# Kernel optimization log

Measured on AMD Instinct MI355X. Metric: run time of the kernel, lower is better.

## Reference

```python
import jax, jax.numpy as jnp
import numpy as np
from jax import lax

B, N, T, D, H, O = 64, 16, 64, 128, 256, 1  # batch, max_neighbors, time_steps, input_dim, hidden_dim, output_dim
NEG = -1e30


def gru(x, h0, Wih, Whh, bih, bhh):
    """Single-layer PyTorch-convention GRU. x:(B,T,D) h0:(B,H) -> (ys:(B,T,H), hT:(B,H))."""
    def step(h, xt):
        gi = xt @ Wih.T + bih          # (B,3H)
        gh = h @ Whh.T + bhh           # (B,3H)
        i_r, i_z, i_n = jnp.split(gi, 3, axis=-1)
        h_r, h_z, h_n = jnp.split(gh, 3, axis=-1)
        r = jax.nn.sigmoid(i_r + h_r)
        z = jax.nn.sigmoid(i_z + h_z)
        n = jnp.tanh(i_n + r * h_n)
        h_new = (1.0 - z) * n + z * h
        return h_new, h_new
    hT, ys = lax.scan(step, h0, jnp.swapaxes(x, 0, 1))
    return jnp.swapaxes(ys, 0, 1), hT


def setup_inputs() -> dict:
    key = jax.random.key(0)
    ks = jax.random.split(key, 16)
    def xavier(k, shape):
        fan_out, fan_in = shape[0], shape[1]
        std = np.sqrt(2.0 / (fan_in + fan_out))
        return jax.random.normal(k, shape, dtype=jnp.float32) * std
    inp = {
        "node_input": jax.random.normal(ks[0], (B, T, D), dtype=jnp.float32),
        "node_hidden": jnp.zeros((1, B, H), dtype=jnp.float32),
        "neighbors_input": jax.random.normal(ks[1], (B, N, T, D), dtype=jnp.float32),
        "neighbors_hidden": jnp.zeros((1, B * N, H), dtype=jnp.float32),
        "s_len": jax.random.randint(ks[2], (B,), 1, T + 1),
        # Node GRU params
        "Wih_node": xavier(ks[3], (3 * H, D)),
        "Whh_node": xavier(ks[4], (3 * H, H)),
        "bih_node": jnp.zeros((3 * H,), dtype=jnp.float32),
        "bhh_node": jnp.zeros((3 * H,), dtype=jnp.float32),
        # Neighbor GRU params
        "Wih_ngh": xavier(ks[5], (3 * H, D)),
        "Whh_ngh": xavier(ks[6], (3 * H, H)),
        "bih_ngh": jnp.zeros((3 * H,), dtype=jnp.float32),
        "bhh_ngh": jnp.zeros((3 * H,), dtype=jnp.float32),
        # Attention projections (torch Linear convention: y = x @ W.T)
        "Wq": xavier(ks[7], (H, H)),
        "Wk": xavier(ks[8], (H, H)),
        "Wv": xavier(ks[9], (H, H)),
        "Wbil": xavier(ks[10], (H, H)),
        "bbil": jnp.zeros((T,), dtype=jnp.float32),
        "Wprj": xavier(ks[11], (O, H)),
        "bprj": jnp.zeros((O,), dtype=jnp.float32),
    }
    return inp


def reference(node_input, node_hidden, neighbors_input, neighbors_hidden, s_len,
              Wih_node, Whh_node, bih_node, bhh_node,
              Wih_ngh, Whh_ngh, bih_ngh, bhh_ngh,
              Wq, Wk, Wv, Wbil, bbil, Wprj, bprj):
    # --- GRU encodes (nlayers=1) ---
    node_out, node_hT = gru(node_input, node_hidden[0], Wih_node, Whh_node, bih_node, bhh_node)  # (B,T,H)
    ngh_in = neighbors_input.reshape(B * N, T, D)
    ngh_out, ngh_hT = gru(ngh_in, neighbors_hidden[0], Wih_ngh, Whh_ngh, bih_ngh, bhh_ngh)
    ngh_out = ngh_out.reshape(B, N, T, H)

    # --- Time attention, batched over all N+1 slots (instead of python loop) ---
    kv = jnp.concatenate([node_out[:, None], ngh_out], axis=1)  # (B,M,T,H), M=N+1
    Q = node_out @ Wq.T                                          # (B,T,H) shared query for all slots
    K = kv @ Wk.T                                                # (B,M,T,H)
    V = kv @ Wv.T                                                # (B,M,T,H)
    # Bilinear score: (Q @ Wbil) @ K^T + b  -> (B,M,T,T); bbil:(T,) broadcasts on last axis
    S = jnp.einsum('bth,bmsh->bmts', Q @ Wbil, K) + bbil
    causal = jnp.triu(jnp.ones((T, T), dtype=bool), k=1)         # mask future positions
    S = jnp.where(causal, NEG, S)
    A = jax.nn.softmax(S, axis=-1)                               # (B,M,T,T); dropout=0 (eval)
    ctx = jnp.einsum('bmts,bmsh->bmth', A, V)                    # (B,M,T,H)

    # --- Output projection and sum over slots ---
    proj = ctx @ Wprj.T + bprj                                   # (B,M,T,O)
    out = jnp.sum(proj.reshape(B, N + 1, T * O), axis=1)         # (B,T*O)
    out = jnp.squeeze(out)
    return out, node_hT[None], ngh_hT[None], A
```

## Files before the change

kernel.cpp:

```cpp
#include <hip/hip_runtime.h>
#include <hip/hip_bf16.h>

#define NEGV -1e30f
typedef __attribute__((ext_vector_type(8))) short bf16x8;
typedef __attribute__((ext_vector_type(4))) float f32x4;

__device__ __forceinline__ float rcpf_(float x) { return __builtin_amdgcn_rcpf(x); }
__device__ __forceinline__ float sigmoidf_(float x) { return rcpf_(1.0f + __expf(-x)); }
__device__ __forceinline__ float tanhf_(float x) {
    float ax = fabsf(x);
    float e = __expf(-2.0f * ax);
    float t = (1.0f - e) * rcpf_(1.0f + e);
    return copysignf(t, x);
}
__device__ __forceinline__ float bf2f(unsigned short u) {
    union { float f; unsigned int i; } x; x.i = ((unsigned int)u) << 16; return x.f;
}
__device__ __forceinline__ float bfsel(uint2 v, int rg) {
    unsigned int w = (rg < 2) ? v.x : v.y;
    return bf2f((unsigned short)((rg & 1) ? (w >> 16) : (w & 0xffffu)));
}

__device__ __forceinline__ void swz_store(const float* __restrict__ src,
    __hip_bfloat16* __restrict__ dst, int idx, int kshift)
{
    int n = idx >> kshift, k = idx & ((1 << kshift) - 1);
    int nt = n >> 4, kt = k >> 5, quad = (k & 31) >> 3, pos = k & 7;
    dst[((size_t)((nt << (kshift - 5)) + kt) * 64 + quad * 16 + (n & 15)) * 8 + pos] =
        (__hip_bfloat16)src[idx];
}

__device__ __forceinline__ void swz_store_g(const float* __restrict__ src,
    __hip_bfloat16* __restrict__ dst, int idx, int kshift)
{
    int n = idx >> kshift, k = idx & ((1 << kshift) - 1);
    int gate = n >> 8, c = n & 255, w = c >> 5, half = (c >> 4) & 1;
    int tileG = w * 6 + gate * 2 + half;
    int kt = k >> 5, quad = (k & 31) >> 3, pos = k & 7;
    dst[((size_t)((tileG << (kshift - 5)) + kt) * 64 + quad * 16 + (n & 15)) * 8 + pos] =
        (__hip_bfloat16)src[idx];
}

__global__ __launch_bounds__(256) void convert_all(
    const float* __restrict__ Wih_n, const float* __restrict__ Wih_g,
    const float* __restrict__ Whh_n, const float* __restrict__ Whh_g,
    const float* __restrict__ Wk_,   const float* __restrict__ Wv_,
    const float* __restrict__ Wbil_, const float* __restrict__ Wq_,
    __hip_bfloat16* Wih_n_sw, __hip_bfloat16* Wih_g_sw,
    __hip_bfloat16* Whh_n_sw, __hip_bfloat16* Whh_g_sw,
    __hip_bfloat16* Wk_sw, __hip_bfloat16* Wv_sw, __hip_bfloat16* wqb_sw)
{
    __shared__ __align__(16) float As[32 * 68];
    __shared__ __align__(16) float Bs[32 * 68];
    if (blockIdx.x < 2816) {
        int g = blockIdx.x * 256 + threadIdx.x;
        if (g < 98304)        swz_store_g(Wih_n, Wih_n_sw, g, 7);
        else if (g < 196608)  swz_store_g(Wih_g, Wih_g_sw, g - 98304, 7);
        else if (g < 393216)  swz_store_g(Whh_n, Whh_n_sw, g - 196608, 8);
        else if (g < 589824)  swz_store_g(Whh_g, Whh_g_sw, g - 393216, 8);
        else if (g < 655360)  swz_store(Wk_,   Wk_sw,   g - 589824, 8);
        else                  swz_store(Wv_,   Wv_sw,   g - 655360, 8);
        return;
    }
    const int bx = blockIdx.x - 2816;
    const int tid = threadIdx.x, tx = tid & 15, ty = tid >> 4;
    const int rb = (bx >> 2) * 64, cb = (bx & 3) * 64;
    float acc[4][4] = {};
    for (int k0 = 0; k0 < 256; k0 += 32) {
        __syncthreads();
        for (int f = tid; f < 2048; f += 256) {
            int kk = f >> 6, r = f & 63;
            As[kk * 68 + r] = Wbil_[(size_t)(k0 + kk) * 256 + rb + r];
        }
        for (int f = tid; f < 2048; f += 256) {
            int kk = f >> 6, c = f & 63;
            Bs[kk * 68 + c] = Wq_[(size_t)(k0 + kk) * 256 + cb + c];
        }
        __syncthreads();
#pragma unroll
        for (int kk = 0; kk < 32; ++kk) {
            float4 a4 = *(const float4*)(As + kk * 68 + ty * 4);
            float4 b4 = *(const float4*)(Bs + kk * 68 + tx * 4);
            float av[4] = {a4.x, a4.y, a4.z, a4.w};
            float bv[4] = {b4.x, b4.y, b4.z, b4.w};
#pragma unroll
            for (int i = 0; i < 4; ++i)
#pragma unroll
                for (int j = 0; j < 4; ++j) acc[i][j] += av[i] * bv[j];
        }
    }
#pragma unroll
    for (int i = 0; i < 4; ++i)
#pragma unroll
        for (int j = 0; j < 4; ++j) {
            int n = rb + ty * 4 + i, k = cb + tx * 4 + j;
            int nt = n >> 4, kt = k >> 5, quad = (k & 31) >> 3, pos = k & 7;
            wqb_sw[((size_t)(nt * 8 + kt) * 64 + quad * 16 + (n & 15)) * 8 + pos] =
                (__hip_bfloat16)acc[i][j];
        }
}

__global__ __launch_bounds__(512) void gi_gemm(
    const float* __restrict__ node_input, const float* __restrict__ neighbors_input,
    const __hip_bfloat16* __restrict__ Wih_n_sw, const __hip_bfloat16* __restrict__ Wih_g_sw,
    const float* __restrict__ bih_node, const float* __restrict__ bhh_node,
    const float* __restrict__ bih_ngh,  const float* __restrict__ bhh_ngh,
    __hip_bfloat16* __restrict__ gi)
{
    __shared__ __align__(16) __hip_bfloat16 xs[64 * 136];
    const int tid = threadIdx.x, wave = tid >> 6, lane = tid & 63;
    const int quad = lane >> 4, lr = lane & 15;
    const int sblk = blockIdx.x >> 4, tc = blockIdx.x & 15;
    const bool isnode = (sblk < 4);
    const float* __restrict__ xb = isnode
        ? (node_input + (size_t)sblk * 16 * 64 * 128)
        : (neighbors_input + ((size_t)sblk * 16 - 64) * 64 * 128);
    const __hip_bfloat16* __restrict__ Wsw = isnode ? Wih_n_sw : Wih_g_sw;
    const float* __restrict__ bi = isnode ? bih_node : bih_ngh;
    const float* __restrict__ bh = isnode ? bhh_node : bhh_ngh;

    bf16x8 wfr[24];
#pragma unroll
    for (int nt = 0; nt < 6; ++nt)
#pragma unroll
        for (int kt = 0; kt < 4; ++kt)
            wfr[nt * 4 + kt] = *(const bf16x8*)(const void*)(
                Wsw + ((size_t)((wave * 6 + nt) * 4 + kt) * 64 + lane) * 8);

    float bias6[6];
#pragma unroll
    for (int tl = 0; tl < 6; ++tl) {
        int gate = tl >> 1;
        int col = gate * 256 + wave * 32 + (tl & 1) * 16 + lr;
        bias6[tl] = bi[col] + (gate < 2 ? bh[col] : 0.0f);
    }

    {
        const int vr = tid >> 3, c0 = (tid & 7) * 16;
        const int r = vr >> 2, tt = vr & 3;
        const float* src = xb + ((size_t)r * 64 + tc * 4 + tt) * 128 + c0;
        float4 v0 = *(const float4*)(src);
        float4 v1 = *(const float4*)(src + 4);
        float4 v2 = *(const float4*)(src + 8);
        float4 v3 = *(const float4*)(src + 12);
        float vv[16] = {v0.x, v0.y, v0.z, v0.w, v1.x, v1.y, v1.z, v1.w,
                        v2.x, v2.y, v2.z, v2.w, v3.x, v3.y, v3.z, v3.w};
        __hip_bfloat16* d = xs + vr * 136 + c0;
#pragma unroll
        for (int j = 0; j < 16; ++j) d[j] = (__hip_bfloat16)vv[j];
    }
    __syncthreads();

    __hip_bfloat16* __restrict__ gout =
        gi + (size_t)((sblk * 8 + wave) * 6) * 16384 + (size_t)lane * 4;

#pragma unroll
    for (int tt = 0; tt < 4; ++tt) {
        int t = tc * 4 + tt;
        bf16x8 afr[4];
#pragma unroll
        for (int kt = 0; kt < 4; ++kt)
            afr[kt] = *(const bf16x8*)(const void*)(xs + (lr * 4 + tt) * 136 + kt * 32 + quad * 8);

#pragma unroll
        for (int tl = 0; tl < 6; ++tl) {
            f32x4 acc = {0.f, 0.f, 0.f, 0.f};
#pragma unroll
            for (int kt = 0; kt < 4; ++kt)
                acc = __builtin_amdgcn_mfma_f32_16x16x32_bf16(afr[kt], wfr[tl * 4 + kt], acc, 0, 0, 0);
            union { __hip_bfloat16 p[4]; uint2 u; } pu;
#pragma unroll
            for (int rg = 0; rg < 4; ++rg) pu.p[rg] = (__hip_bfloat16)(acc[rg] + bias6[tl]);
            *(uint2*)(void*)(gout + (size_t)tl * 16384 + (size_t)t * 256) = pu.u;
        }
    }
}

__global__ __launch_bounds__(512, 2) void scan_kernel(
    const __hip_bfloat16* __restrict__ gi,
    const __hip_bfloat16* __restrict__ Whh_n_sw,
    const __hip_bfloat16* __restrict__ Whh_g_sw,
    const float* __restrict__ bhh_node, const float* __restrict__ bhh_ngh,
    const float* __restrict__ node_hidden, const float* __restrict__ neighbors_hidden,
    __hip_bfloat16* __restrict__ node_out, __hip_bfloat16* __restrict__ ngh_out,
    float* __restrict__ out_node_hT, float* __restrict__ out_ngh_hT)
{
    __shared__ __align__(16) __hip_bfloat16 wlds[96 * 64 * 8];
    __shared__ __align__(16) __hip_bfloat16 hfr[2 * 4096];
    const int tid = threadIdx.x;
    const int wave = tid >> 6, lane = tid & 63;
    const int quad = lane >> 4, lr = lane & 15;
    const int row0 = blockIdx.x * 16;
    const bool isnode = (row0 < 64);
    const __hip_bfloat16* __restrict__ Wsw = isnode ? Whh_n_sw : Whh_g_sw;
    const float* __restrict__ bhh = isnode ? bhh_node : bhh_ngh;

    bf16x8 wreg[36];
#pragma unroll
    for (int nt = 0; nt < 6; ++nt)
#pragma unroll
        for (int kt = 0; kt < 6; ++kt)
            wreg[nt * 6 + kt] = *(const bf16x8*)(const void*)(
                Wsw + ((size_t)((wave * 6 + nt) * 8 + kt) * 64 + lane) * 8);

    for (int f = tid; f < 6144; f += 512) {
        int chunk = f >> 6, l = f & 63;
        int tileG = chunk >> 1, s = chunk & 1;
        *(uint4*)(void*)(wlds + ((size_t)chunk * 64 + l) * 8) =
            *(const uint4*)(const void*)(Wsw + ((size_t)(tileG * 8 + 6 + s) * 64 + l) * 8);
    }

    const __hip_bfloat16* __restrict__ gbase =
        gi + (size_t)((blockIdx.x * 8 + wave) * 6) * 16384 + (size_t)lane * 4;

    const float bhn0 = bhh[512 + wave * 32 + lr];
    const float bhn1 = bhh[512 + wave * 32 + 16 + lr];

    const int hwoff = (wave * 64 + (lr >> 3) * 16 + quad * 4) * 8 + (lr & 7);
    float hreg[8];
    {
        const float* hsrc = isnode ? (node_hidden + (size_t)row0 * 256)
                                   : (neighbors_hidden + (size_t)(row0 - 64) * 256);
#pragma unroll
        for (int half = 0; half < 2; ++half)
#pragma unroll
            for (int rg = 0; rg < 4; ++rg) {
                float v = hsrc[(size_t)(quad * 4 + rg) * 256 + wave * 32 + half * 16 + lr];
                hreg[half * 4 + rg] = v;
                hfr[hwoff + half * 256 + rg * 8] = (__hip_bfloat16)v;
            }
    }

    __hip_bfloat16* optr;
    {
        int orow = tid & 15;
        int ocol = (tid >> 6) * 32 + ((tid >> 4) & 3) * 8;
        optr = isnode ? (node_out + ((size_t)(row0 + orow) * 64) * 256 + ocol)
                      : (ngh_out + ((size_t)(row0 - 64 + orow) * 64) * 256 + ocol);
    }

    uint2 gv[6];
#pragma unroll
    for (int tl = 0; tl < 6; ++tl)
        gv[tl] = *(const uint2*)(const void*)(gbase + (size_t)tl * 16384);

    __syncthreads();

#pragma unroll 1
    for (int t = 0; t < 64; ++t) {
        const __hip_bfloat16* hr = hfr + (t & 1) * 4096;

        const int tp = (t < 63) ? (t + 1) : 63;
        uint2 gvn[6];
#pragma unroll
        for (int tl = 0; tl < 6; ++tl)
            gvn[tl] = *(const uint2*)(const void*)(gbase + (size_t)tl * 16384 + tp * 256);

        if (t) {
            uint4 ov = *(const uint4*)(const void*)(hr + tid * 8);
            *(uint4*)(void*)optr = ov;
            optr += 256;
        }

        f32x4 acc[6] = {{0.f,0.f,0.f,0.f},{0.f,0.f,0.f,0.f},{0.f,0.f,0.f,0.f},
                        {0.f,0.f,0.f,0.f},{0.f,0.f,0.f,0.f},{0.f,0.f,0.f,0.f}};
        {
#pragma unroll
            for (int kt = 0; kt < 3; ++kt) {
                bf16x8 av = *(const bf16x8*)(const void*)(hr + (kt * 64 + lane) * 8);
#pragma unroll
                for (int tl = 0; tl < 6; ++tl)
                    acc[tl] = __builtin_amdgcn_mfma_f32_16x16x32_bf16(av, wreg[tl * 6 + kt], acc[tl], 0, 0, 0);
            }
        }
        {
#pragma unroll
            for (int kt = 3; kt < 6; ++kt) {
                bf16x8 av = *(const bf16x8*)(const void*)(hr + (kt * 64 + lane) * 8);
#pragma unroll
                for (int tl = 0; tl < 6; ++tl)
                    acc[tl] = __builtin_amdgcn_mfma_f32_16x16x32_bf16(av, wreg[tl * 6 + kt], acc[tl], 0, 0, 0);
            }
        }
        {
#pragma unroll
            for (int s = 0; s < 2; ++s) {
                bf16x8 av = *(const bf16x8*)(const void*)(hr + ((6 + s) * 64 + lane) * 8);
#pragma unroll
                for (int tl = 0; tl < 6; ++tl) {
                    bf16x8 bfr = *(const bf16x8*)(const void*)(
                        wlds + ((size_t)((wave * 6 + tl) * 2 + s) * 64 + lane) * 8);
                    acc[tl] = __builtin_amdgcn_mfma_f32_16x16x32_bf16(av, bfr, acc[tl], 0, 0, 0);
                }
            }
        }

        __hip_bfloat16* hw = hfr + ((t + 1) & 1) * 4096 + hwoff;
#pragma unroll
        for (int half = 0; half < 2; ++half) {
            const float bhn = half ? bhn1 : bhn0;
#pragma unroll
            for (int rg = 0; rg < 4; ++rg) {
                float ghr = acc[half][rg];
                float ghz = acc[2 + half][rg];
                float ghn = acc[4 + half][rg] + bhn;
                float gir = bfsel(gv[half], rg);
                float giz = bfsel(gv[2 + half], rg);
                float gin = bfsel(gv[4 + half], rg);
                float r = sigmoidf_(gir + ghr);
                float z = sigmoidf_(giz + ghz);
                float n = tanhf_(gin + r * ghn);
                float hn = (1.0f - z) * n + z * hreg[half * 4 + rg];
                hreg[half * 4 + rg] = hn;
                hw[half * 256 + rg * 8] = (__hip_bfloat16)hn;
            }
        }
#pragma unroll
        for (int tl = 0; tl < 6; ++tl) gv[tl] = gvn[tl];

        asm volatile("s_waitcnt lgkmcnt(0)" ::: "memory");
        __builtin_amdgcn_s_barrier();
        __builtin_amdgcn_sched_barrier(0);
    }

    {
        uint4 ov = *(const uint4*)(const void*)(hfr + tid * 8);
        *(uint4*)(void*)optr = ov;
    }
    {
        float* hdst = isnode ? (out_node_hT + (size_t)row0 * 256)
                             : (out_ngh_hT + (size_t)(row0 - 64) * 256);
#pragma unroll
        for (int half = 0; half < 2; ++half)
#pragma unroll
            for (int rg = 0; rg < 4; ++rg)
                hdst[(size_t)(quad * 4 + rg) * 256 + wave * 32 + half * 16 + lr] = hreg[half * 4 + rg];
    }
}

__global__ __launch_bounds__(256) void q_gemm(
    const __hip_bfloat16* __restrict__ A0,
    const __hip_bfloat16* __restrict__ wqb_sw,
    __hip_bfloat16* __restrict__ Qb)
{
    __shared__ __align__(16) __hip_bfloat16 As[64 * 264];
    const int tid = threadIdx.x, wave = tid >> 6, lane = tid & 63;
    const int quad = lane >> 4, lr = lane & 15;
    const int rb = blockIdx.x * 64;
    const __hip_bfloat16* A = A0 + (size_t)rb * 256;

    for (int f = tid; f < 2048; f += 256) {
        int row = f >> 5, cc = (f & 31) * 8;
        *(uint4*)(void*)(As + row * 264 + cc) =
            *(const uint4*)(const void*)(A + (size_t)row * 256 + cc);
    }
    __syncthreads();

    bf16x8 afr[8];
#pragma unroll
    for (int kt = 0; kt < 8; ++kt)
        afr[kt] = *(const bf16x8*)(const void*)(As + (wave * 16 + lr) * 264 + kt * 32 + quad * 8);

    const int s0 = wave * 16 + quad * 4;
    for (int ntg = 0; ntg < 16; ++ntg) {
        f32x4 acc = {0.f, 0.f, 0.f, 0.f};
#pragma unroll
        for (int kt = 0; kt < 8; ++kt) {
            bf16x8 bfr = *(const bf16x8*)(const void*)(wqb_sw + ((size_t)(ntg * 8 + kt) * 64 + lane) * 8);
            acc = __builtin_amdgcn_mfma_f32_16x16x32_bf16(afr[kt], bfr, acc, 0, 0, 0);
        }
        int col = ntg * 16 + lr;
#pragma unroll
        for (int rg = 0; rg < 4; ++rg)
            Qb[(size_t)(rb + s0 + rg) * 256 + col] = (__hip_bfloat16)acc[rg];
    }
}

__global__ __launch_bounds__(256) void attn_fused(
    const __hip_bfloat16* __restrict__ node_out_b,
    const __hip_bfloat16* __restrict__ ngh_out_b,
    const __hip_bfloat16* __restrict__ Wk_sw, const __hip_bfloat16* __restrict__ Wv_sw,
    const __hip_bfloat16* __restrict__ Qb, const float* __restrict__ bbil,
    const float* __restrict__ Wprj, const float* __restrict__ bprj,
    float* __restrict__ A_out, float* __restrict__ out)
{
    __shared__ __align__(16) __hip_bfloat16 KA[64 * 264];
    __shared__ __align__(16) float Sbuf[64 * 68];
    __shared__ __align__(16) __hip_bfloat16 Pb[64 * 72];
    __shared__ float rowmax[64], rowrcp[64];
    __shared__ float red[64 * 16];
    const int tid = threadIdx.x;
    const int wave = tid >> 6, lane = tid & 63;
    const int quad = lane >> 4, lr = lane & 15;
    const int bm = blockIdx.x, b = bm / 17, m = bm % 17;
    const __hip_bfloat16* __restrict__ A = (m == 0)
        ? (node_out_b + (size_t)b * 64 * 256)
        : (ngh_out_b + ((size_t)(b * 16 + m - 1) * 64) * 256);

    for (int f = tid; f < 2048; f += 256) {
        int row = f >> 5, cc = (f & 31) * 8;
        *(uint4*)(void*)(KA + row * 264 + cc) =
            *(const uint4*)(const void*)(A + (size_t)row * 256 + cc);
    }
    __syncthreads();

    bf16x8 afr[8];
#pragma unroll
    for (int kt = 0; kt < 8; ++kt)
        afr[kt] = *(const bf16x8*)(const void*)(KA + (wave * 16 + lr) * 264 + kt * 32 + quad * 8);
    const __hip_bfloat16* Qrow = Qb + (size_t)b * 64 * 256;
    bf16x8 qfr[8];
#pragma unroll
    for (int kt = 0; kt < 8; ++kt)
        qfr[kt] = *(const bf16x8*)(const void*)(Qrow + (size_t)(wave * 16 + lr) * 256 + kt * 32 + quad * 8);
    __syncthreads();

    {
        const int s0 = wave * 16 + quad * 4;
        for (int ntg = 0; ntg < 16; ++ntg) {
            f32x4 acc = {0.f, 0.f, 0.f, 0.f};
#pragma unroll
            for (int kt = 0; kt < 8; ++kt) {
                bf16x8 bfr = *(const bf16x8*)(const void*)(Wk_sw + ((size_t)(ntg * 8 + kt) * 64 + lane) * 8);
                acc = __builtin_amdgcn_mfma_f32_16x16x32_bf16(afr[kt], bfr, acc, 0, 0, 0);
            }
            int col = ntg * 16 + lr;
#pragma unroll
            for (int rg = 0; rg < 4; ++rg)
                KA[(s0 + rg) * 264 + col] = (__hip_bfloat16)acc[rg];
        }
    }
    __syncthreads();

    f32x4 sacc[4] = {{0.f,0.f,0.f,0.f},{0.f,0.f,0.f,0.f},{0.f,0.f,0.f,0.f},{0.f,0.f,0.f,0.f}};
#pragma unroll
    for (int kt = 0; kt < 8; ++kt) {
#pragma unroll
        for (int c = 0; c < 4; ++c) {
            bf16x8 bfr = *(const bf16x8*)(const void*)(KA + (c * 16 + lr) * 264 + kt * 32 + quad * 8);
            sacc[c] = __builtin_amdgcn_mfma_f32_16x16x32_bf16(qfr[kt], bfr, sacc[c], 0, 0, 0);
        }
    }
#pragma unroll
    for (int c = 0; c < 4; ++c)
#pragma unroll
        for (int rg = 0; rg < 4; ++rg) {
            int t_ = wave * 16 + quad * 4 + rg, s_ = c * 16 + lr;
            Sbuf[t_ * 68 + s_] = (s_ <= t_) ? (sacc[c][rg] + bbil[s_]) : NEGV;
        }
    __syncthreads();

    {
        const int kt2 = wave >> 1;
        const int lp = ((wave & 1) * 2 + (quad >> 1)) * 16 + lr;
        const int j0 = (quad & 1) * 4;
        for (int ntg = 0; ntg < 16; ++ntg) {
            f32x4 acc = {0.f, 0.f, 0.f, 0.f};
#pragma unroll
            for (int kt = 0; kt < 8; ++kt) {
                bf16x8 bfr = *(const bf16x8*)(const void*)(Wv_sw + ((size_t)(ntg * 8 + kt) * 64 + lane) * 8);
                acc = __builtin_amdgcn_mfma_f32_16x16x32_bf16(afr[kt], bfr, acc, 0, 0, 0);
            }
            __hip_bfloat16 t4[4];
#pragma unroll
            for (int rg = 0; rg < 4; ++rg) t4[rg] = (__hip_bfloat16)acc[rg];
            *(uint2*)(void*)(KA + (size_t)(((ntg * 2 + kt2) * 64 + lp) * 8 + j0)) =
                *(const uint2*)(const void*)t4;
        }
    }
    if (tid < 64) {
        float mx = -3.0e38f;
        for (int s = 0; s < 64; ++s) mx = fmaxf(mx, Sbuf[tid * 68 + s]);
        float sum = 0.0f;
        for (int s = 0; s < 64; ++s) sum += __expf(Sbuf[tid * 68 + s] - mx);
        rowmax[tid] = mx;
        rowrcp[tid] = 1.0f / sum;
    }
    __syncthreads();

    for (int idx = tid; idx < 4096; idx += 256) {
        int t_ = idx >> 6, s_ = idx & 63;
        float e = __expf(Sbuf[t_ * 68 + s_] - rowmax[t_]) * rowrcp[t_];
        A_out[(size_t)bm * 4096 + idx] = e;
        Pb[t_ * 72 + s_] = (__hip_bfloat16)e;
    }
    __syncthreads();

    bf16x8 pfr[2];
#pragma unroll
    for (int k2 = 0; k2 < 2; ++k2)
        pfr[k2] = *(const bf16x8*)(const void*)(Pb + (wave * 16 + lr) * 72 + k2 * 32 + quad * 8);
    float part[4] = {0.f, 0.f, 0.f, 0.f};
#pragma unroll
    for (int nt = 0; nt < 16; ++nt) {
        f32x4 cacc = {0.f, 0.f, 0.f, 0.f};
#pragma unroll
        for (int k2 = 0; k2 < 2; ++k2) {
            bf16x8 bfr = *(const bf16x8*)(const void*)(KA + (size_t)((nt * 2 + k2) * 64 + lane) * 8);
            cacc = __builtin_amdgcn_mfma_f32_16x16x32_bf16(pfr[k2], bfr, cacc, 0, 0, 0);
        }
        float wp = Wprj[nt * 16 + lr];
#pragma unroll
        for (int rg = 0; rg < 4; ++rg) part[rg] += cacc[rg] * wp;
    }
#pragma unroll
    for (int rg = 0; rg < 4; ++rg) red[(wave * 16 + quad * 4 + rg) * 16 + lr] = part[rg];
    __syncthreads();
    if (tid < 64) {
        float s = 0.0f;
#pragma unroll
        for (int q = 0; q < 16; ++q) s += red[tid * 16 + q];
        if (m == 0) s += 17.0f * bprj[0];
        atomicAdd(out + b * 64 + tid, s);
    }
}

extern "C" void kernel_launch(void* const* d_in, const int* in_sizes, int n_in,
                              void* d_out, int out_size, void* d_ws, size_t ws_size,
                              hipStream_t stream)
{
    const float* node_input       = (const float*)d_in[0];
    const float* node_hidden      = (const float*)d_in[1];
    const float* neighbors_input  = (const float*)d_in[2];
    const float* neighbors_hidden = (const float*)d_in[3];
    const float* Wih_node = (const float*)d_in[5];
    const float* Whh_node = (const float*)d_in[6];
    const float* bih_node = (const float*)d_in[7];
    const float* bhh_node = (const float*)d_in[8];
    const float* Wih_ngh  = (const float*)d_in[9];
    const float* Whh_ngh  = (const float*)d_in[10];
    const float* bih_ngh  = (const float*)d_in[11];
    const float* bhh_ngh  = (const float*)d_in[12];
    const float* Wq   = (const float*)d_in[13];
    const float* Wk   = (const float*)d_in[14];
    const float* Wv   = (const float*)d_in[15];
    const float* Wbil = (const float*)d_in[16];
    const float* bbil = (const float*)d_in[17];
    const float* Wprj = (const float*)d_in[18];
    const float* bprj = (const float*)d_in[19];

    float* out         = (float*)d_out;
    float* out_node_hT = out + 4096;
    float* out_ngh_hT  = out + 20480;
    float* out_A       = out + 282624;

    char* w = (char*)d_ws;
    __hip_bfloat16* Wih_n_sw = (__hip_bfloat16*)(w + 262144);
    __hip_bfloat16* Wih_g_sw = (__hip_bfloat16*)(w + 458752);
    __hip_bfloat16* Whh_n_sw = (__hip_bfloat16*)(w + 655360);
    __hip_bfloat16* Whh_g_sw = (__hip_bfloat16*)(w + 1048576);
    __hip_bfloat16* Wk_sw    = (__hip_bfloat16*)(w + 1441792);
    __hip_bfloat16* Wv_sw    = (__hip_bfloat16*)(w + 1572864);
    __hip_bfloat16* wqb_sw   = (__hip_bfloat16*)(w + 1703936);
    __hip_bfloat16* node_out_b = (__hip_bfloat16*)(w + 1835008);
    __hip_bfloat16* ngh_out_b  = (__hip_bfloat16*)(w + 3932160);
    __hip_bfloat16* qb_b       = (__hip_bfloat16*)(w + 37486592);
    __hip_bfloat16* gi         = (__hip_bfloat16*)(w + 39583744);

    hipMemsetAsync(d_out, 0, 4096 * sizeof(float), stream);

    convert_all<<<2832, 256, 0, stream>>>(
        Wih_node, Wih_ngh, Whh_node, Whh_ngh, Wk, Wv, Wbil, Wq,
        Wih_n_sw, Wih_g_sw, Whh_n_sw, Whh_g_sw, Wk_sw, Wv_sw, wqb_sw);

    gi_gemm<<<1088, 512, 0, stream>>>(
        node_input, neighbors_input, Wih_n_sw, Wih_g_sw,
        bih_node, bhh_node, bih_ngh, bhh_ngh, gi);

    scan_kernel<<<68, 512, 0, stream>>>(gi, Whh_n_sw, Whh_g_sw,
        bhh_node, bhh_ngh, node_hidden, neighbors_hidden,
        node_out_b, ngh_out_b, out_node_hT, out_ngh_hT);

    q_gemm<<<64, 256, 0, stream>>>(node_out_b, wqb_sw, qb_b);

    attn_fused<<<1088, 256, 0, stream>>>(
        node_out_b, ngh_out_b, Wk_sw, Wv_sw, qb_b, bbil, Wprj, bprj,
        out_A, out);
}
```

Measured before the change: 393.9 us.

## Fold Wk into query side so attention skips per-slot K projection

After: 413.1 us. +4.9%, slower.

```diff
diff --git a/kernel.cpp b/kernel.cpp
--- a/kernel.cpp
+++ b/kernel.cpp
@@ -48,7 +48,8 @@
     const float* __restrict__ Wbil_, const float* __restrict__ Wq_,
     __hip_bfloat16* Wih_n_sw, __hip_bfloat16* Wih_g_sw,
     __hip_bfloat16* Whh_n_sw, __hip_bfloat16* Whh_g_sw,
-    __hip_bfloat16* Wk_sw, __hip_bfloat16* Wv_sw, __hip_bfloat16* wqb_sw)
+    __hip_bfloat16* Wk_sw, __hip_bfloat16* Wv_sw, __hip_bfloat16* wqb_sw,
+    __hip_bfloat16* Wk_t_sw)
 {
     __shared__ __align__(16) float As[32 * 68];
     __shared__ __align__(16) float Bs[32 * 68];
@@ -62,7 +63,16 @@
         else                  swz_store(Wv_,   Wv_sw,   g - 655360, 8);
         return;
     }
-    const int bx = blockIdx.x - 2816;
+    if (blockIdx.x < 3072) {
+        int g = (blockIdx.x - 2816) * 256 + threadIdx.x;
+        int k = g >> 8, n = g & 255;
+        float v = Wk_[(size_t)k * 256 + n];
+        int nt = n >> 4, kt = k >> 5, quad = (k & 31) >> 3, pos = k & 7;
+        Wk_t_sw[((size_t)(nt * 8 + kt) * 64 + quad * 16 + (n & 15)) * 8 + pos] =
+            (__hip_bfloat16)v;
+        return;
+    }
+    const int bx = blockIdx.x - 3072;
     const int tid = threadIdx.x, tx = tid & 15, ty = tid >> 4;
     const int rb = (bx >> 2) * 64, cb = (bx & 3) * 64;
     float acc[4][4] = {};
@@ -341,7 +351,8 @@
 __global__ __launch_bounds__(256) void q_gemm(
     const __hip_bfloat16* __restrict__ A0,
     const __hip_bfloat16* __restrict__ wqb_sw,
-    __hip_bfloat16* __restrict__ Qb)
+    const __hip_bfloat16* __restrict__ Wk_t_sw,
+    __hip_bfloat16* __restrict__ G)
 {
     __shared__ __align__(16) __hip_bfloat16 As[64 * 264];
     const int tid = threadIdx.x, wave = tid >> 6, lane = tid & 63;
@@ -360,6 +371,7 @@
 #pragma unroll
     for (int kt = 0; kt < 8; ++kt)
         afr[kt] = *(const bf16x8*)(const void*)(As + (wave * 16 + lr) * 264 + kt * 32 + quad * 8);
+    __syncthreads();
 
     const int s0 = wave * 16 + quad * 4;
     for (int ntg = 0; ntg < 16; ++ntg) {
@@ -372,15 +384,33 @@
         int col = ntg * 16 + lr;
 #pragma unroll
         for (int rg = 0; rg < 4; ++rg)
-            Qb[(size_t)(rb + s0 + rg) * 256 + col] = (__hip_bfloat16)acc[rg];
+            As[(s0 + rg) * 264 + col] = (__hip_bfloat16)acc[rg];
+    }
+    __syncthreads();
+
+    bf16x8 qfr[8];
+#pragma unroll
+    for (int kt = 0; kt < 8; ++kt)
+        qfr[kt] = *(const bf16x8*)(const void*)(As + (wave * 16 + lr) * 264 + kt * 32 + quad * 8);
+    for (int ntg = 0; ntg < 16; ++ntg) {
+        f32x4 acc = {0.f, 0.f, 0.f, 0.f};
+#pragma unroll
+        for (int kt = 0; kt < 8; ++kt) {
+            bf16x8 bfr = *(const bf16x8*)(const void*)(Wk_t_sw + ((size_t)(ntg * 8 + kt) * 64 + lane) * 8);
+            acc = __builtin_amdgcn_mfma_f32_16x16x32_bf16(qfr[kt], bfr, acc, 0, 0, 0);
+        }
+        int col = ntg * 16 + lr;
+#pragma unroll
+        for (int rg = 0; rg < 4; ++rg)
+            G[(size_t)(rb + s0 + rg) * 256 + col] = (__hip_bfloat16)acc[rg];
     }
 }
 
 __global__ __launch_bounds__(256) void attn_fused(
     const __hip_bfloat16* __restrict__ node_out_b,
     const __hip_bfloat16* __restrict__ ngh_out_b,
-    const __hip_bfloat16* __restrict__ Wk_sw, const __hip_bfloat16* __restrict__ Wv_sw,
-    const __hip_bfloat16* __restrict__ Qb, const float* __restrict__ bbil,
+    const __hip_bfloat16* __restrict__ Wv_sw,
+    const __hip_bfloat16* __restrict__ G, const float* __restrict__ bbil,
     const float* __restrict__ Wprj, const float* __restrict__ bprj,
     float* __restrict__ A_out, float* __restrict__ out)
 {
@@ -408,29 +438,11 @@
 #pragma unroll
     for (int kt = 0; kt < 8; ++kt)
         afr[kt] = *(const bf16x8*)(const void*)(KA + (wave * 16 + lr) * 264 + kt * 32 + quad * 8);
-    const __hip_bfloat16* Qrow = Qb + (size_t)b * 64 * 256;
-    bf16x8 qfr[8];
+    const __hip_bfloat16* Grow = G + (size_t)b * 64 * 256;
+    bf16x8 gfr[8];
 #pragma unroll
     for (int kt = 0; kt < 8; ++kt)
-        qfr[kt] = *(const bf16x8*)(const void*)(Qrow + (size_t)(wave * 16 + lr) * 256 + kt * 32 + quad * 8);
-    __syncthreads();
-
-    {
-        const int s0 = wave * 16 + quad * 4;
-        for (int ntg = 0; ntg < 16; ++ntg) {
-            f32x4 acc = {0.f, 0.f, 0.f, 0.f};
-#pragma unroll
-            for (int kt = 0; kt < 8; ++kt) {
-                bf16x8 bfr = *(const bf16x8*)(const void*)(Wk_sw + ((size_t)(ntg * 8 + kt) * 64 + lane) * 8);
-                acc = __builtin_amdgcn_mfma_f32_16x16x32_bf16(afr[kt], bfr, acc, 0, 0, 0);
-            }
-            int col = ntg * 16 + lr;
-#pragma unroll
-            for (int rg = 0; rg < 4; ++rg)
-                KA[(s0 + rg) * 264 + col] = (__hip_bfloat16)acc[rg];
-        }
-    }
-    __syncthreads();
+        gfr[kt] = *(const bf16x8*)(const void*)(Grow + (size_t)(wave * 16 + lr) * 256 + kt * 32 + quad * 8);
 
     f32x4 sacc[4] = {{0.f,0.f,0.f,0.f},{0.f,0.f,0.f,0.f},{0.f,0.f,0.f,0.f},{0.f,0.f,0.f,0.f}};
 #pragma unroll
@@ -438,7 +450,7 @@
 #pragma unroll
         for (int c = 0; c < 4; ++c) {
             bf16x8 bfr = *(const bf16x8*)(const void*)(KA + (c * 16 + lr) * 264 + kt * 32 + quad * 8);
-            sacc[c] = __builtin_amdgcn_mfma_f32_16x16x32_bf16(qfr[kt], bfr, sacc[c], 0, 0, 0);
+            sacc[c] = __builtin_amdgcn_mfma_f32_16x16x32_bf16(gfr[kt], bfr, sacc[c], 0, 0, 0);
         }
     }
 #pragma unroll
@@ -545,6 +557,7 @@
     float* out_A       = out + 282624;
 
     char* w = (char*)d_ws;
+    __hip_bfloat16* Wk_t_sw  = (__hip_bfloat16*)(w);
     __hip_bfloat16* Wih_n_sw = (__hip_bfloat16*)(w + 262144);
     __hip_bfloat16* Wih_g_sw = (__hip_bfloat16*)(w + 458752);
     __hip_bfloat16* Whh_n_sw = (__hip_bfloat16*)(w + 655360);
@@ -554,14 +567,14 @@
     __hip_bfloat16* wqb_sw   = (__hip_bfloat16*)(w + 1703936);
     __hip_bfloat16* node_out_b = (__hip_bfloat16*)(w + 1835008);
     __hip_bfloat16* ngh_out_b  = (__hip_bfloat16*)(w + 3932160);
-    __hip_bfloat16* qb_b       = (__hip_bfloat16*)(w + 37486592);
+    __hip_bfloat16* g_b        = (__hip_bfloat16*)(w + 37486592);
     __hip_bfloat16* gi         = (__hip_bfloat16*)(w + 39583744);
 
     hipMemsetAsync(d_out, 0, 4096 * sizeof(float), stream);
 
-    convert_all<<<2832, 256, 0, stream>>>(
+    convert_all<<<3088, 256, 0, stream>>>(
         Wih_node, Wih_ngh, Whh_node, Whh_ngh, Wk, Wv, Wbil, Wq,
-        Wih_n_sw, Wih_g_sw, Whh_n_sw, Whh_g_sw, Wk_sw, Wv_sw, wqb_sw);
+        Wih_n_sw, Wih_g_sw, Whh_n_sw, Whh_g_sw, Wk_sw, Wv_sw, wqb_sw, Wk_t_sw);
 
     gi_gemm<<<1088, 512, 0, stream>>>(
         node_input, neighbors_input, Wih_n_sw, Wih_g_sw,
@@ -571,9 +584,9 @@
         bhh_node, bhh_ngh, node_hidden, neighbors_hidden,
         node_out_b, ngh_out_b, out_node_hT, out_ngh_hT);
 
-    q_gemm<<<64, 256, 0, stream>>>(node_out_b, wqb_sw, qb_b);
+    q_gemm<<<64, 256, 0, stream>>>(node_out_b, wqb_sw, Wk_t_sw, g_b);
 
     attn_fused<<<1088, 256, 0, stream>>>(
-        node_out_b, ngh_out_b, Wk_sw, Wv_sw, qb_b, bbil, Wprj, bprj,
+        node_out_b, ngh_out_b, Wv_sw, g_b, bbil, Wprj, bprj,
         out_A, out);
 }
```
